# Kernel tuning notes

Measured on AMD Instinct MI355X. Metric: run time of the kernel, lower is better.

The kernel has to match this reference:

```python
import jax, jax.numpy as jnp
import numpy as np

_K = 256  # d_model // 8


def setup_inputs() -> dict:
    key = jax.random.key(0)
    ks = jax.random.split(key, 7)
    B, T, D = 4, 4096, 2048
    x = jax.random.normal(ks[0], (B, T, D), jnp.float32)
    ema_mean = 0.1 * jax.random.normal(ks[1], (D,), jnp.float32)
    # ensure positive variance: ema_sq - ema_mean^2 in [0.5, 1.5]
    ema_sq = ema_mean ** 2 + 0.5 + jax.random.uniform(ks[2], (D,), jnp.float32)
    ema_out = jax.random.normal(ks[3], (D,), jnp.float32)
    log_tau = 0.1 * jax.random.normal(ks[4], (), jnp.float32)
    log_sigma_raw = 0.1 * jax.random.normal(ks[5], (), jnp.float32)
    log_w_raw = 0.1 * jax.random.normal(ks[6], (), jnp.float32)
    return {
        "x": x,
        "ema_mean": ema_mean,
        "ema_sq": ema_sq,
        "ema_out": ema_out,
        "log_tau": log_tau,
        "log_sigma_raw": log_sigma_raw,
        "log_w_raw": log_w_raw,
    }


def reference(x, ema_mean, ema_sq, ema_out, log_tau, log_sigma_raw, log_w_raw):
    tau = jnp.exp(log_tau)
    sigma = jax.nn.softplus(log_sigma_raw) + 0.01
    w = jax.nn.softplus(log_w_raw)

    out = jax.nn.gelu(x, approximate=False)  # F.gelu default = exact erf

    # z-score against EMA stats
    std = jnp.sqrt(jnp.clip(ema_sq - ema_mean ** 2, 1e-6, None))
    z = (x - ema_mean) / std

    # topk |z| over channel dim, gather z, mean of |z_topk|
    _, idx = jax.lax.top_k(jnp.abs(z), _K)          # idx: [B,T,K]
    z_topk = jnp.take_along_axis(z, idx, axis=-1)
    topk_mean = jnp.mean(jnp.abs(z_topk), axis=-1, keepdims=True)  # [B,T,1]
    surp = jnp.tanh(sigma * topk_mean)

    # cosine similarity of gelu output against EMA output direction
    ema_u = ema_out / (jnp.linalg.norm(ema_out) + 1e-8)
    out_n = out / jnp.maximum(
        jnp.linalg.norm(out, axis=-1, keepdims=True), 1e-12
    )  # F.normalize eps
    cos_out = jnp.sum(out_n * ema_u, axis=-1, keepdims=True)  # [B,T,1]

    gate = jnp.exp(-tau * cos_out) * (1.0 + w * surp)
    return out * gate
```

## Files before the change

kernel.cpp:

```cpp
#include <hip/hip_runtime.h>
#include <math.h>

#define D      2048
#define KSEL   256
#define NT     256
#define NBINS  512
#define ROWS   2

typedef float f4 __attribute__((ext_vector_type(4)));
typedef int   i4 __attribute__((ext_vector_type(4)));

__device__ __forceinline__ float fast_gelu(float x) {
    float x2 = x * x;
    float t  = fmaf(x2, -0.0713548162f, -1.5957691216f);
    float e  = __expf(x * t);
    return x * __builtin_amdgcn_rcpf(1.0f + e);
}

template<int CTRL, int RMASK>
__device__ __forceinline__ float dpp_mov_f(float v) {
    int r = __builtin_amdgcn_update_dpp(0, __builtin_bit_cast(int, v),
                                        CTRL, RMASK, 0xf, true);
    return __builtin_bit_cast(float, r);
}
template<int CTRL, int RMASK>
__device__ __forceinline__ int dpp_mov_i(int v) {
    return __builtin_amdgcn_update_dpp(0, v, CTRL, RMASK, 0xf, true);
}
__device__ __forceinline__ float wave_scan_f(float x) {
    x += dpp_mov_f<0x111, 0xf>(x);
    x += dpp_mov_f<0x112, 0xf>(x);
    x += dpp_mov_f<0x114, 0xf>(x);
    x += dpp_mov_f<0x118, 0xf>(x);
    x += dpp_mov_f<0x142, 0xa>(x);
    x += dpp_mov_f<0x143, 0xc>(x);
    return x;
}
__device__ __forceinline__ int wave_scan_i(int x) {
    x += dpp_mov_i<0x111, 0xf>(x);
    x += dpp_mov_i<0x112, 0xf>(x);
    x += dpp_mov_i<0x114, 0xf>(x);
    x += dpp_mov_i<0x118, 0xf>(x);
    x += dpp_mov_i<0x142, 0xa>(x);
    x += dpp_mov_i<0x143, 0xc>(x);
    return x;
}

__global__ __launch_bounds__(NT) void row_kernel(
    const float* __restrict__ x,
    const float* __restrict__ ema_mean,
    const float* __restrict__ ema_sq,
    const float* __restrict__ ema_out,
    const float* __restrict__ p_log_tau,
    const float* __restrict__ p_log_sigma,
    const float* __restrict__ p_log_w,
    float* __restrict__ out)
{
    __shared__ int   hist[NBINS];
    __shared__ float ssred[4];
    __shared__ float red[4][3];
    __shared__ int   bsel_sh, krem_sh;

    const int t    = threadIdx.x;
    const int wave = t >> 6;
    const int lane = t & 63;

    const float tau   = __expf(p_log_tau[0]);
    const float sigma = __logf(1.0f + __expf(p_log_sigma[0])) + 0.01f;
    const float w     = __logf(1.0f + __expf(p_log_w[0]));

    f4 m0 = ((const f4*)ema_mean)[t];
    f4 m1 = ((const f4*)ema_mean)[t + NT];
    f4 q0 = ((const f4*)ema_sq)[t];
    f4 q1 = ((const f4*)ema_sq)[t + NT];
    f4 e0 = ((const f4*)ema_out)[t];
    f4 e1 = ((const f4*)ema_out)[t + NT];

    const float mv[8] = {m0.x,m0.y,m0.z,m0.w, m1.x,m1.y,m1.z,m1.w};
    const float qv[8] = {q0.x,q0.y,q0.z,q0.w, q1.x,q1.y,q1.z,q1.w};
    const float ev[8] = {e0.x,e0.y,e0.z,e0.w, e1.x,e1.y,e1.z,e1.w};

    float a_[8], b_[8];
    float ss = 0.f;
#pragma unroll
    for (int j = 0; j < 8; ++j) {
        float v = fmaxf(fmaf(-mv[j], mv[j], qv[j]), 1e-6f);
        a_[j] = 64.0f * __builtin_amdgcn_rsqf(v);
        b_[j] = -mv[j] * a_[j];
        ss = fmaf(ev[j], ev[j], ss);
    }
    ss = wave_scan_f(ss);
    if (lane == 63) ssred[wave] = ss;

    const size_t row0 = (size_t)blockIdx.x * ROWS;
    f4 xa = ((const f4*)(x + row0 * D))[t];
    f4 xb = ((const f4*)(x + row0 * D))[t + NT];

    hist[t] = 0;
    hist[t + NT] = 0;
    __syncthreads();

    const float inv_nrm =
        1.0f / (sqrtf(ssred[0] + ssred[1] + ssred[2] + ssred[3]) + 1e-8f);
    float u_[8];
#pragma unroll
    for (int j = 0; j < 8; ++j) u_[j] = ev[j] * inv_nrm;

#pragma unroll
    for (int r = 0; r < ROWS; ++r) {
        const float xv[8] = {xa.x,xa.y,xa.z,xa.w, xb.x,xb.y,xb.z,xb.w};

        float g[8], av[8];
        float dot = 0.f, nrm = 0.f;
#pragma unroll
        for (int j = 0; j < 8; ++j) {
            float gg = fast_gelu(xv[j]);
            g[j] = gg;
            av[j] = fabsf(fmaf(xv[j], a_[j], b_[j]));
            dot = fmaf(gg, u_[j], dot);
            nrm = fmaf(gg, gg, nrm);
        }

        if (r + 1 < ROWS) {
            const float* xn = x + (row0 + r + 1) * D;
            xa = ((const f4*)xn)[t];
            xb = ((const f4*)xn)[t + NT];
        }

#pragma unroll
        for (int j = 0; j < 8; ++j) {
            int bin = (int)av[j];
            bin = bin > NBINS - 1 ? NBINS - 1 : bin;
            atomicAdd(&hist[(NBINS - 1) - bin], 1);
        }
        __syncthreads();

        if (wave == 0) {
            i4 va = *(const i4*)&hist[8 * lane];
            i4 vb = *(const i4*)&hist[8 * lane + 4];
            int c0 = va.x;
            int c1 = c0 + va.y;
            int c2 = c1 + va.z;
            int c3 = c2 + va.w;
            int c4 = c3 + vb.x;
            int c5 = c4 + vb.y;
            int c6 = c5 + vb.z;
            int c7 = c6 + vb.w;
            int incl = wave_scan_i(c7);
            int excl = incl - c7;
            int pre[8] = {0, c0, c1, c2, c3, c4, c5, c6};
            int cum[8] = {c0, c1, c2, c3, c4, c5, c6, c7};
#pragma unroll
            for (int k = 0; k < 8; ++k) {
                int s0 = excl + pre[k];
                int e0x = excl + cum[k];
                if (s0 < KSEL && e0x >= KSEL) {
                    bsel_sh = (NBINS - 1) - (8 * lane + k);
                    krem_sh = KSEL - s0;
                }
            }
        }
        __syncthreads();

        const int   bsel = bsel_sh;
        const int   krem = krem_sh;
        const float hi  = (bsel == NBINS - 1) ? __builtin_inff() : (float)(bsel + 1);
        const float mid = (float)bsel + 0.5f;

        float s = 0.f;
#pragma unroll
        for (int j = 0; j < 8; ++j) {
            s += (av[j] >= hi) ? av[j] : 0.f;
        }

        dot = wave_scan_f(dot);
        nrm = wave_scan_f(nrm);
        s   = wave_scan_f(s);
        if (lane == 63) {
            red[wave][0] = dot; red[wave][1] = nrm; red[wave][2] = s;
        }
        hist[t] = 0;
        hist[t + NT] = 0;
        __syncthreads();

        dot = red[0][0] + red[1][0] + red[2][0] + red[3][0];
        nrm = red[0][1] + red[1][1] + red[2][1] + red[3][1];
        s   = red[0][2] + red[1][2] + red[2][2] + red[3][2];

        const float topk_mean = (s + (float)krem * mid) * (1.0f / (64.0f * KSEL));
        const float cosv = dot * __builtin_amdgcn_rsqf(fmaxf(nrm, 1e-24f));
        const float yt = sigma * topk_mean;
        const float et = __expf(-2.0f * yt);
        const float th = (1.0f - et) * __builtin_amdgcn_rcpf(1.0f + et);
        const float gate = __expf(-tau * cosv) * fmaf(w, th, 1.0f);

        f4 oa, ob;
        oa.x = g[0]*gate; oa.y = g[1]*gate; oa.z = g[2]*gate; oa.w = g[3]*gate;
        ob.x = g[4]*gate; ob.y = g[5]*gate; ob.z = g[6]*gate; ob.w = g[7]*gate;
        f4* outr = (f4*)(out + (row0 + r) * D);
        outr[t]      = oa;
        outr[t + NT] = ob;
    }
}

extern "C" void kernel_launch(void* const* d_in, const int* in_sizes, int n_in,
                              void* d_out, int out_size, void* d_ws, size_t ws_size,
                              hipStream_t stream) {
    (void)n_in; (void)out_size; (void)d_ws; (void)ws_size;
    const float* x         = (const float*)d_in[0];
    const float* ema_mean  = (const float*)d_in[1];
    const float* ema_sq    = (const float*)d_in[2];
    const float* ema_out   = (const float*)d_in[3];
    const float* log_tau   = (const float*)d_in[4];
    const float* log_sigma = (const float*)d_in[5];
    const float* log_w     = (const float*)d_in[6];
    float* out = (float*)d_out;

    const int rows = in_sizes[0] / D;
    row_kernel<<<rows / ROWS, NT, 0, stream>>>(x, ema_mean, ema_sq, ema_out,
                                               log_tau, log_sigma, log_w, out);
}
```

Before: 45.84 us.

## Double-buffer histogram and compute top-k threshold per wave to drop barrier

```diff
diff --git a/kernel.cpp b/kernel.cpp
--- a/kernel.cpp
+++ b/kernel.cpp
@@ -5,7 +5,7 @@
 #define KSEL   256
 #define NT     256
 #define NBINS  512
-#define ROWS   2
+#define ROWS   4
 
 typedef float f4 __attribute__((ext_vector_type(4)));
 typedef int   i4 __attribute__((ext_vector_type(4)));
@@ -43,6 +43,15 @@
     x += dpp_mov_i<0x118, 0xf>(x);
     x += dpp_mov_i<0x142, 0xa>(x);
     x += dpp_mov_i<0x143, 0xc>(x);
+    return x;
+}
+__device__ __forceinline__ int wave_or_i(int x) {
+    x |= dpp_mov_i<0x111, 0xf>(x);
+    x |= dpp_mov_i<0x112, 0xf>(x);
+    x |= dpp_mov_i<0x114, 0xf>(x);
+    x |= dpp_mov_i<0x118, 0xf>(x);
+    x |= dpp_mov_i<0x142, 0xa>(x);
+    x |= dpp_mov_i<0x143, 0xc>(x);
     return x;
 }
 
@@ -56,10 +65,9 @@
     const float* __restrict__ p_log_w,
     float* __restrict__ out)
 {
-    __shared__ int   hist[NBINS];
+    __shared__ int   hist[2][NBINS];
     __shared__ float ssred[4];
     __shared__ float red[4][3];
-    __shared__ int   bsel_sh, krem_sh;
 
     const int t    = threadIdx.x;
     const int wave = t >> 6;
@@ -96,8 +104,8 @@
     f4 xa = ((const f4*)(x + row0 * D))[t];
     f4 xb = ((const f4*)(x + row0 * D))[t + NT];
 
-    hist[t] = 0;
-    hist[t + NT] = 0;
+    hist[0][t] = 0;  hist[0][t + NT] = 0;
+    hist[1][t] = 0;  hist[1][t + NT] = 0;
     __syncthreads();
 
     const float inv_nrm =
@@ -108,6 +116,7 @@
 
 #pragma unroll
     for (int r = 0; r < ROWS; ++r) {
+        const int p = r & 1;
         const float xv[8] = {xa.x,xa.y,xa.z,xa.w, xb.x,xb.y,xb.z,xb.w};
 
         float g[8], av[8];
@@ -127,17 +136,24 @@
             xb = ((const f4*)xn)[t + NT];
         }
 
+        dot = wave_scan_f(dot);
+        nrm = wave_scan_f(nrm);
+        if (lane == 63) { red[wave][0] = dot; red[wave][1] = nrm; }
+
 #pragma unroll
         for (int j = 0; j < 8; ++j) {
             int bin = (int)av[j];
             bin = bin > NBINS - 1 ? NBINS - 1 : bin;
-            atomicAdd(&hist[(NBINS - 1) - bin], 1);
+            atomicAdd(&hist[p][(NBINS - 1) - bin], 1);
         }
         __syncthreads();
 
-        if (wave == 0) {
-            i4 va = *(const i4*)&hist[8 * lane];
-            i4 vb = *(const i4*)&hist[8 * lane + 4];
+        int enc;
+        {
+            i4 va = *(const i4*)&hist[p][8 * lane];
+            i4 vb = *(const i4*)&hist[p][8 * lane + 4];
+            hist[p ^ 1][t] = 0;
+            hist[p ^ 1][t + NT] = 0;
             int c0 = va.x;
             int c1 = c0 + va.y;
             int c2 = c1 + va.z;
@@ -148,22 +164,21 @@
             int c7 = c6 + vb.w;
             int incl = wave_scan_i(c7);
             int excl = incl - c7;
-            int pre[8] = {0, c0, c1, c2, c3, c4, c5, c6};
-            int cum[8] = {c0, c1, c2, c3, c4, c5, c6, c7};
+            const int pre[8] = {0, c0, c1, c2, c3, c4, c5, c6};
+            const int cum[8] = {c0, c1, c2, c3, c4, c5, c6, c7};
+            enc = 0;
 #pragma unroll
             for (int k = 0; k < 8; ++k) {
                 int s0 = excl + pre[k];
                 int e0x = excl + cum[k];
-                if (s0 < KSEL && e0x >= KSEL) {
-                    bsel_sh = (NBINS - 1) - (8 * lane + k);
-                    krem_sh = KSEL - s0;
-                }
+                if (s0 < KSEL && e0x >= KSEL)
+                    enc = ((NBINS - 1) - (8 * lane + k)) | ((KSEL - s0) << 16);
             }
-        }
-        __syncthreads();
-
-        const int   bsel = bsel_sh;
-        const int   krem = krem_sh;
+            enc = wave_or_i(enc);
+            enc = __builtin_amdgcn_readlane(enc, 63);
+        }
+        const int   bsel = enc & 0xffff;
+        const int   krem = enc >> 16;
         const float hi  = (bsel == NBINS - 1) ? __builtin_inff() : (float)(bsel + 1);
         const float mid = (float)bsel + 0.5f;
 
@@ -172,15 +187,8 @@
         for (int j = 0; j < 8; ++j) {
             s += (av[j] >= hi) ? av[j] : 0.f;
         }
-
-        dot = wave_scan_f(dot);
-        nrm = wave_scan_f(nrm);
-        s   = wave_scan_f(s);
-        if (lane == 63) {
-            red[wave][0] = dot; red[wave][1] = nrm; red[wave][2] = s;
-        }
-        hist[t] = 0;
-        hist[t + NT] = 0;
+        s = wave_scan_f(s);
+        if (lane == 63) red[wave][2] = s;
         __syncthreads();
 
         dot = red[0][0] + red[1][0] + red[2][0] + red[3][0];
```

New measurement: 48.14 us. 5.0% more time.

## Compute top-k sum redundantly per wave from histogram, drop extra barriers

Applied to the files above, without the earlier changes.

```diff
diff --git a/kernel.cpp b/kernel.cpp
--- a/kernel.cpp
+++ b/kernel.cpp
@@ -44,6 +44,10 @@
     x += dpp_mov_i<0x142, 0xa>(x);
     x += dpp_mov_i<0x143, 0xc>(x);
     return x;
+}
+__device__ __forceinline__ float wave_bcast63_f(float x) {
+    int r = __builtin_amdgcn_readlane(__builtin_bit_cast(int, x), 63);
+    return __builtin_bit_cast(float, r);
 }
 
 __global__ __launch_bounds__(NT) void row_kernel(
@@ -56,10 +60,9 @@
     const float* __restrict__ p_log_w,
     float* __restrict__ out)
 {
-    __shared__ int   hist[NBINS];
+    __shared__ int   hist[ROWS][NBINS];
     __shared__ float ssred[4];
-    __shared__ float red[4][3];
-    __shared__ int   bsel_sh, krem_sh;
+    __shared__ float red[ROWS][4][2];
 
     const int t    = threadIdx.x;
     const int wave = t >> 6;
@@ -96,8 +99,8 @@
     f4 xa = ((const f4*)(x + row0 * D))[t];
     f4 xb = ((const f4*)(x + row0 * D))[t + NT];
 
-    hist[t] = 0;
-    hist[t + NT] = 0;
+    hist[0][t] = 0;  hist[0][t + NT] = 0;
+    hist[1][t] = 0;  hist[1][t + NT] = 0;
     __syncthreads();
 
     const float inv_nrm =
@@ -127,67 +130,63 @@
             xb = ((const f4*)xn)[t + NT];
         }
 
+        dot = wave_scan_f(dot);
+        nrm = wave_scan_f(nrm);
+        if (lane == 63) { red[r][wave][0] = dot; red[r][wave][1] = nrm; }
+
 #pragma unroll
         for (int j = 0; j < 8; ++j) {
             int bin = (int)av[j];
             bin = bin > NBINS - 1 ? NBINS - 1 : bin;
-            atomicAdd(&hist[(NBINS - 1) - bin], 1);
+            atomicAdd(&hist[r][(NBINS - 1) - bin], 1);
         }
         __syncthreads();
 
-        if (wave == 0) {
-            i4 va = *(const i4*)&hist[8 * lane];
-            i4 vb = *(const i4*)&hist[8 * lane + 4];
-            int c0 = va.x;
-            int c1 = c0 + va.y;
-            int c2 = c1 + va.z;
-            int c3 = c2 + va.w;
-            int c4 = c3 + vb.x;
-            int c5 = c4 + vb.y;
-            int c6 = c5 + vb.z;
-            int c7 = c6 + vb.w;
-            int incl = wave_scan_i(c7);
-            int excl = incl - c7;
-            int pre[8] = {0, c0, c1, c2, c3, c4, c5, c6};
-            int cum[8] = {c0, c1, c2, c3, c4, c5, c6, c7};
+        i4 va = *(const i4*)&hist[r][8 * lane];
+        i4 vb = *(const i4*)&hist[r][8 * lane + 4];
+        const float base = 511.5f - (float)(8 * lane);
+        int c0 = va.x;
+        int c1 = c0 + va.y;
+        int c2 = c1 + va.z;
+        int c3 = c2 + va.w;
+        int c4 = c3 + vb.x;
+        int c5 = c4 + vb.y;
+        int c6 = c5 + vb.z;
+        int c7 = c6 + vb.w;
+        float w0 = (float)va.x * base;
+        float w1 = fmaf((float)va.y, base - 1.0f, w0);
+        float w2 = fmaf((float)va.z, base - 2.0f, w1);
+        float w3 = fmaf((float)va.w, base - 3.0f, w2);
+        float w4 = fmaf((float)vb.x, base - 4.0f, w3);
+        float w5 = fmaf((float)vb.y, base - 5.0f, w4);
+        float w6 = fmaf((float)vb.z, base - 6.0f, w5);
+        float w7 = fmaf((float)vb.w, base - 7.0f, w6);
+
+        int   incl  = wave_scan_i(c7);
+        int   excl  = incl - c7;
+        float winc  = wave_scan_f(w7);
+        float wexcl = winc - w7;
+
+        float ts = 0.f;
+        {
+            const int   pre[8]  = {0, c0, c1, c2, c3, c4, c5, c6};
+            const int   cum[8]  = {c0, c1, c2, c3, c4, c5, c6, c7};
+            const float wpre[8] = {0.f, w0, w1, w2, w3, w4, w5, w6};
 #pragma unroll
             for (int k = 0; k < 8; ++k) {
-                int s0 = excl + pre[k];
+                int s0  = excl + pre[k];
                 int e0x = excl + cum[k];
-                if (s0 < KSEL && e0x >= KSEL) {
-                    bsel_sh = (NBINS - 1) - (8 * lane + k);
-                    krem_sh = KSEL - s0;
-                }
+                if (s0 < KSEL && e0x >= KSEL)
+                    ts = fmaf((float)(KSEL - s0), base - (float)k,
+                              wexcl + wpre[k]);
             }
         }
-        __syncthreads();
-
-        const int   bsel = bsel_sh;
-        const int   krem = krem_sh;
-        const float hi  = (bsel == NBINS - 1) ? __builtin_inff() : (float)(bsel + 1);
-        const float mid = (float)bsel + 0.5f;
-
-        float s = 0.f;
-#pragma unroll
-        for (int j = 0; j < 8; ++j) {
-            s += (av[j] >= hi) ? av[j] : 0.f;
-        }
-
-        dot = wave_scan_f(dot);
-        nrm = wave_scan_f(nrm);
-        s   = wave_scan_f(s);
-        if (lane == 63) {
-            red[wave][0] = dot; red[wave][1] = nrm; red[wave][2] = s;
-        }
-        hist[t] = 0;
-        hist[t + NT] = 0;
-        __syncthreads();
-
-        dot = red[0][0] + red[1][0] + red[2][0] + red[3][0];
-        nrm = red[0][1] + red[1][1] + red[2][1] + red[3][1];
-        s   = red[0][2] + red[1][2] + red[2][2] + red[3][2];
-
-        const float topk_mean = (s + (float)krem * mid) * (1.0f / (64.0f * KSEL));
+        ts = wave_bcast63_f(wave_scan_f(ts));
+
+        dot = red[r][0][0] + red[r][1][0] + red[r][2][0] + red[r][3][0];
+        nrm = red[r][0][1] + red[r][1][1] + red[r][2][1] + red[r][3][1];
+
+        const float topk_mean = ts * (1.0f / (64.0f * KSEL));
         const float cosv = dot * __builtin_amdgcn_rsqf(fmaxf(nrm, 1e-24f));
         const float yt = sigma * topk_mean;
         const float et = __expf(-2.0f * yt);
```

Result: slower. 47.09 us (+2.7%).
